# Kernel optimization log

Hardware: AMD Instinct MI355X
Metric: run time of the kernel (lower is better)

## Reference

```python
import jax, jax.numpy as jnp
import numpy as np

D_MODEL = 192
D_INNER = 384          # expand(2) * d_model
HEADDIM = 12
NHEADS = 32            # d_inner // headdim
DSTATE = 16
NGROUPS = 1
CONV_DIM = D_INNER + 2 * NGROUPS * DSTATE          # 416
D_IN_PROJ = 2 * D_INNER + 2 * NGROUPS * DSTATE + NHEADS  # 832
LN_EPS = 1e-5


def silu(x):
    return x * jax.nn.sigmoid(x)


def depthwise_conv2d(x_nchw, w, b):
    # groups == channels depthwise conv, kernel 3, padding 1 (SAME)
    out = jax.lax.conv_general_dilated(
        x_nchw, w, window_strides=(1, 1), padding='SAME',
        feature_group_count=CONV_DIM,
        dimension_numbers=('NCHW', 'OIHW', 'NCHW'))
    return out + b[None, :, None, None]


def setup_inputs() -> dict:
    key = jax.random.key(0)
    ks = jax.random.split(key, 10)
    Bn, H, W = 4, 128, 128
    u = jax.random.normal(ks[0], (Bn, H, W, D_MODEL), jnp.float32)
    t = jax.random.normal(ks[1], (Bn, H, W, D_MODEL), jnp.float32)
    s_in = 1.0 / np.sqrt(D_MODEL)
    W_in = jax.random.normal(ks[2], (D_IN_PROJ, D_MODEL), jnp.float32) * s_in
    W_t_in = jax.random.normal(ks[3], (D_IN_PROJ, D_MODEL), jnp.float32) * s_in
    conv_w = jax.random.normal(ks[4], (CONV_DIM, 1, 3, 3), jnp.float32) * (1.0 / 3.0)
    conv_b = jnp.zeros((CONV_DIM,), jnp.float32)
    # dt_bias = inverse-softplus of dt sampled log-uniform in [dt_min, dt_max]
    dt0 = jnp.exp(jax.random.uniform(ks[5], (NHEADS,)) * (np.log(0.1) - np.log(0.001)) + np.log(0.001))
    dt_bias = dt0 + jnp.log(-jnp.expm1(-dt0))
    A_log = jnp.log(jax.random.uniform(ks[6], (NHEADS,), minval=1.0, maxval=16.0))
    D = jnp.ones((NHEADS,), jnp.float32)
    ln_gamma = jnp.ones((D_INNER,), jnp.float32)
    ln_beta = jnp.zeros((D_INNER,), jnp.float32)
    W_out = jax.random.normal(ks[7], (D_MODEL, D_INNER), jnp.float32) * (1.0 / np.sqrt(D_INNER))
    return dict(u=u, t=t, W_in=W_in, W_t_in=W_t_in, conv_w=conv_w, conv_b=conv_b,
                dt_bias=dt_bias, A_log=A_log, D=D, ln_gamma=ln_gamma, ln_beta=ln_beta,
                W_out=W_out)


def reference(u, t, W_in, W_t_in, conv_w, conv_b, dt_bias, A_log, D,
              ln_gamma, ln_beta, W_out):
    B0, H, W_, C0 = u.shape
    L = H * W_
    uu = u.reshape(B0, L, C0)
    tt = t.reshape(B0, L, C0)

    # in_proj on main branch: split into z, xBC, dt
    zxbcdt = uu @ W_in.T                                    # (B, L, 832)
    z = zxbcdt[..., :D_INNER]                               # (B, L, 384)
    xBC = zxbcdt[..., D_INNER:D_INNER + CONV_DIM]           # (B, L, 416)
    dt = zxbcdt[..., D_INNER + CONV_DIM:]                   # (B, L, 32)
    dt = jax.nn.softplus(dt + dt_bias)

    # t branch: only x1B1C1 part is ultimately used (C := C1)
    x1B1C1 = (tt @ W_t_in.T)[..., D_INNER:D_INNER + CONV_DIM]

    # depthwise 3x3 conv + silu on both branches
    xBC = xBC.reshape(B0, H, W_, CONV_DIM).transpose(0, 3, 1, 2)
    xBC = silu(depthwise_conv2d(xBC, conv_w, conv_b))
    xBC = xBC.transpose(0, 2, 3, 1).reshape(B0, L, CONV_DIM)

    x1B1C1 = x1B1C1.reshape(B0, H, W_, CONV_DIM).transpose(0, 3, 1, 2)
    x1B1C1 = silu(depthwise_conv2d(x1B1C1, conv_w, conv_b))
    x1B1C1 = x1B1C1.transpose(0, 2, 3, 1).reshape(B0, L, CONV_DIM)

    x = xBC[..., :D_INNER]                                  # V features (B, L, 384)
    Bk = xBC[..., D_INNER:D_INNER + NGROUPS * DSTATE]       # K (B, L, 16)
    Cq = x1B1C1[..., D_INNER + NGROUPS * DSTATE:]           # Q from t-branch (B, L, 16)

    A = -jnp.exp(A_log)                                     # (nheads,), negative

    # non-causal linear attention duality (ngroups == 1)
    V = x.reshape(B0, L, NHEADS, HEADDIM).transpose(0, 2, 1, 3)   # (B, h, L, d)
    dtT = dt.transpose(0, 2, 1)                                   # (B, h, L)
    dA = -(dtT[..., None] * A[None, :, None, None])               # ssd_positve_dA: positive
    V_scaled = V * dA
    KV = jnp.einsum('bln,bhld->bhnd', Bk, V_scaled)               # (B, h, 16, 12)
    y = jnp.einsum('bln,bhnd->bhld', Cq, KV) + V * D[None, :, None, None]
    y = y.transpose(0, 2, 1, 3).reshape(B0, L, D_INNER)

    # LayerNorm over d_inner
    mu = jnp.mean(y, axis=-1, keepdims=True)
    var = jnp.mean((y - mu) ** 2, axis=-1, keepdims=True)
    y = (y - mu) * jax.lax.rsqrt(var + LN_EPS) * ln_gamma + ln_beta

    y = y * z
    out = y @ W_out.T
    return out.reshape(B0, H, W_, C0)
```

## Files before the change

kernel.cpp:

```cpp
#include <hip/hip_runtime.h>
#include <hip/hip_bf16.h>
#include <math.h>


#define BN 4
#define HH 128
#define WWID 128
#define LTOK (HH*WWID)
#define NTOK (BN*LTOK)
#define DMODEL 192
#define DINNER 384
#define NH 32
#define HD 12
#define DST 16
#define CONVD 416
#define KVCHUNKS 64
#define PM 256
#define TILE_SH 12288
#define TILE_BY 24576
#define TROW ((size_t)NTOK*64)

typedef __hip_bfloat16 bf16;
typedef unsigned int uint32;
typedef unsigned short ushort16;
typedef __attribute__((ext_vector_type(8))) short bf16x8;
typedef __attribute__((ext_vector_type(4))) float f32x4;
typedef __attribute__((ext_vector_type(16))) float f32x16;

__device__ __forceinline__ float bflo(uint32 v){ return __uint_as_float((v & 0xffffu) << 16); }
__device__ __forceinline__ float bfhi(uint32 v){ return __uint_as_float(v & 0xffff0000u); }
__device__ __forceinline__ ushort16 f2bf(float f){
    __hip_bfloat16 h = __float2bfloat16(f);
    return *reinterpret_cast<const ushort16*>(&h);
}
__device__ __forceinline__ float ldbf(const bf16* p){
    return __uint_as_float(((uint32)(*(const ushort16*)p)) << 16);
}
__device__ __forceinline__ float softplusf(float x){
    return (x > 20.f) ? x : log1pf(expf(x));
}
__device__ __forceinline__ float siluf(float x){
    return x / (1.f + expf(-x));
}

union BFPK { short s[8]; bf16x8 v; };

__global__ __launch_bounds__(256) void k_prep(
    const float* __restrict__ Win, const float* __restrict__ Wout,
    const float* __restrict__ cw,
    bf16* __restrict__ Wsw, bf16* __restrict__ Woutbf, float* __restrict__ wtr)
{
    const int i = blockIdx.x*256 + threadIdx.x;
    if (i < 832*DMODEL) {
        const int ch = i / DMODEL, k = i - ch*DMODEL;
        const int nt = ch >> 6, row = ch & 63;
        const int ks = k ^ ((row & 7) << 3);
        Wsw[(size_t)nt*TILE_SH + row*DMODEL + ks] = __float2bfloat16(Win[i]);
    }
    if (i < DMODEL*DINNER) Woutbf[i] = __float2bfloat16(Wout[i]);
    if (i < CONVD*9) { const int c = i/9, k = i - c*9; wtr[k*420 + c] = cw[i]; }
}

__global__ __launch_bounds__(512) void k_proj_mfma(
    const float* __restrict__ u, const bf16* __restrict__ Wsw,
    const float* __restrict__ dt_b, const float* __restrict__ A_log,
    bf16* __restrict__ z_bf, bf16* __restrict__ xbc_pre, float* __restrict__ dA)
{
    __shared__ __align__(16) short S[3*TILE_SH];

    const int tid = threadIdx.x;
    const int m0 = blockIdx.x * PM;
    const int ntbase = blockIdx.y * 7;
    const int ntiles = blockIdx.y ? 6 : 7;
    const int wid = tid >> 6, lane = tid & 63;
    const int fr = lane & 31;
    const int hi = lane >> 5;

    const char* gW = (const char*)Wsw;
    auto GLOAD = [&](int nt, int buf) {
        const char* src = gW + (size_t)nt*TILE_BY + wid*3072 + lane*16;
        char* dst = ((char*)S) + buf*TILE_BY + wid*3072;
        #pragma unroll
        for (int c = 0; c < 3; ++c)
            __builtin_amdgcn_global_load_lds(
                (const __attribute__((address_space(1))) void*)(src + c*1024),
                (__attribute__((address_space(3))) void*)(dst + c*1024), 16, 0, 0);
    };

    GLOAD(ntbase, 0);

    const float db = dt_b[fr];
    const float al = expf(A_log[fr]);
    bf16x8 a[12];
    {
        const float* arow = u + (size_t)(m0 + wid*32 + fr)*DMODEL;
        #pragma unroll
        for (int ks=0;ks<12;++ks) {
            const float4 a0 = *(const float4*)(arow + ks*16 + hi*8);
            const float4 a1 = *(const float4*)(arow + ks*16 + hi*8 + 4);
            BFPK pk;
            pk.s[0]=(short)f2bf(a0.x); pk.s[1]=(short)f2bf(a0.y);
            pk.s[2]=(short)f2bf(a0.z); pk.s[3]=(short)f2bf(a0.w);
            pk.s[4]=(short)f2bf(a1.x); pk.s[5]=(short)f2bf(a1.y);
            pk.s[6]=(short)f2bf(a1.z); pk.s[7]=(short)f2bf(a1.w);
            a[ks] = pk.v;
        }
    }
    asm volatile("s_waitcnt vmcnt(0)" ::: "memory");
    GLOAD(ntbase + 1, 1);
    __builtin_amdgcn_s_barrier();
    __builtin_amdgcn_sched_barrier(0);

    const int kswz = (fr & 7) << 3;

    for (int i = 0; i < ntiles; ++i) {
        const int nt = ntbase + i;
        const short* Sb = &S[(i % 3)*TILE_SH];

        f32x16 acc0, acc1;
        #pragma unroll
        for (int q=0;q<16;++q) { acc0[q]=0.f; acc1[q]=0.f; }

        #pragma unroll
        for (int ks=0;ks<12;++ks) {
            const int kk = (ks*16 + hi*8) ^ kswz;
            const bf16x8 b0 = *(const bf16x8*)&Sb[fr*DMODEL + kk];
            const bf16x8 b1 = *(const bf16x8*)&Sb[(32+fr)*DMODEL + kk];
            acc0 = __builtin_amdgcn_mfma_f32_32x32x16_bf16(a[ks], b0, acc0, 0, 0, 0);
            acc1 = __builtin_amdgcn_mfma_f32_32x32x16_bf16(a[ks], b1, acc1, 0, 0, 0);
        }

        #pragma unroll
        for (int ni=0;ni<2;++ni) {
            const f32x16& ac = ni ? acc1 : acc0;
            const int n0 = nt*64 + ni*32;
            if (n0 < DINNER) {
                bf16* dst = z_bf + (size_t)nt*TROW + (ni*32 + fr);
                #pragma unroll
                for (int r=0;r<16;++r) {
                    const int tok = m0 + wid*32 + (r&3) + 8*(r>>2) + 4*hi;
                    dst[(size_t)tok*64] = __float2bfloat16(ac[r]);
                }
            } else if (n0 < 800) {
                const int loc = n0 - DINNER + fr;
                bf16* dst = xbc_pre + (size_t)(loc>>6)*TROW + (loc & 63);
                #pragma unroll
                for (int r=0;r<16;++r) {
                    const int tok = m0 + wid*32 + (r&3) + 8*(r>>2) + 4*hi;
                    dst[(size_t)tok*64] = __float2bfloat16(ac[r]);
                }
            } else {
                #pragma unroll
                for (int r=0;r<16;++r) {
                    const int tok = m0 + wid*32 + (r&3) + 8*(r>>2) + 4*hi;
                    const float dt = softplusf(ac[r] + db);
                    dA[(size_t)tok*NH + fr] = dt * al;
                }
            }
        }

        if (i + 2 < ntiles) {
            GLOAD(nt + 2, (i + 2) % 3);
            asm volatile("s_waitcnt vmcnt(35)" ::: "memory");
        } else {
            asm volatile("s_waitcnt vmcnt(32)" ::: "memory");
        }
        __builtin_amdgcn_s_barrier();
        __builtin_amdgcn_sched_barrier(0);
    }
}

__global__ __launch_bounds__(256) void k_tproj(
    const float* __restrict__ t, const float* __restrict__ Wtin, float* __restrict__ cq_pre)
{
    __shared__ float ts[16][196];
    __shared__ float ws[16][196];
    const int tid = threadIdx.x;
    const int tok0 = blockIdx.x * 16;
    #pragma unroll
    for (int i = 0; i < 3; ++i) {
        const int flat = tid + 256*i;
        const int row = flat / 48, c = (flat % 48)*4;
        *(float4*)&ts[row][c] = *(const float4*)(t    + (size_t)(tok0+row)*DMODEL + c);
        *(float4*)&ws[row][c] = *(const float4*)(Wtin + (size_t)(784+row)*DMODEL + c);
    }
    __syncthreads();
    const int tt = tid >> 4, n = tid & 15;
    float s0=0.f,s1=0.f,s2=0.f,s3=0.f;
    #pragma unroll 4
    for (int k = 0; k < DMODEL; k += 4) {
        s0 = fmaf(ts[tt][k+0], ws[n][k+0], s0);
        s1 = fmaf(ts[tt][k+1], ws[n][k+1], s1);
        s2 = fmaf(ts[tt][k+2], ws[n][k+2], s2);
        s3 = fmaf(ts[tt][k+3], ws[n][k+3], s3);
    }
    cq_pre[(size_t)(tok0+tt)*DST + n] = (s0+s1)+(s2+s3);
}

__global__ __launch_bounds__(416) void k_conv416(
    const bf16* __restrict__ in, const float* __restrict__ wtr, const float* __restrict__ cb,
    bf16* __restrict__ out)
{
    __shared__ float ws[9*420];
    __shared__ float bs[416];
    const int tid = threadIdx.x;
    for (int i = tid; i < 9*420; i += 416) ws[i] = wtr[i];
    if (tid < 416) bs[tid] = cb[tid];
    __syncthreads();

    const int pl  = tid / 52;
    const int grp = tid - pl*52;
    const int c0  = grp*8;
    const int pix = blockIdx.x*8 + pl;
    const int hw  = pix & (LTOK-1);
    const int h = hw >> 7, w = hw & 127;
    const int bb = pix >> 14;

    const bf16* inT = in + (size_t)(c0 >> 6)*TROW + (c0 & 63);

    float acc[8];
    {
        const float4 b0 = *(const float4*)&bs[c0];
        const float4 b1 = *(const float4*)&bs[c0+4];
        acc[0]=b0.x; acc[1]=b0.y; acc[2]=b0.z; acc[3]=b0.w;
        acc[4]=b1.x; acc[5]=b1.y; acc[6]=b1.z; acc[7]=b1.w;
    }

    #pragma unroll
    for (int dh=-1; dh<=1; ++dh) {
        const int hh = h + dh;
        if ((unsigned)hh >= (unsigned)HH) continue;
        #pragma unroll
        for (int dw=-1; dw<=1; ++dw) {
            const int w2 = w + dw;
            if ((unsigned)w2 >= (unsigned)WWID) continue;
            const int wi = (dh+1)*3 + (dw+1);
            const int pix2 = (bb<<14) + (hh<<7) + w2;
            const uint4 v = *(const uint4*)((const ushort16*)inT + (size_t)pix2*64);
            const float4 w0 = *(const float4*)&ws[wi*420 + c0];
            const float4 w1 = *(const float4*)&ws[wi*420 + c0 + 4];
            acc[0] = fmaf(bflo(v.x), w0.x, acc[0]);
            acc[1] = fmaf(bfhi(v.x), w0.y, acc[1]);
            acc[2] = fmaf(bflo(v.y), w0.z, acc[2]);
            acc[3] = fmaf(bfhi(v.y), w0.w, acc[3]);
            acc[4] = fmaf(bflo(v.z), w1.x, acc[4]);
            acc[5] = fmaf(bfhi(v.z), w1.y, acc[5]);
            acc[6] = fmaf(bflo(v.w), w1.z, acc[6]);
            acc[7] = fmaf(bfhi(v.w), w1.w, acc[7]);
        }
    }

    uint4 o;
    o.x = ((uint32)f2bf(siluf(acc[1])) << 16) | (uint32)f2bf(siluf(acc[0]));
    o.y = ((uint32)f2bf(siluf(acc[3])) << 16) | (uint32)f2bf(siluf(acc[2]));
    o.z = ((uint32)f2bf(siluf(acc[5])) << 16) | (uint32)f2bf(siluf(acc[4]));
    o.w = ((uint32)f2bf(siluf(acc[7])) << 16) | (uint32)f2bf(siluf(acc[6]));
    *(uint4*)((ushort16*)out + (size_t)pix*CONVD + c0) = o;
}

__global__ __launch_bounds__(256) void k_conv16(
    const float* __restrict__ in, const float* __restrict__ cw, const float* __restrict__ cb,
    bf16* __restrict__ out)
{
    const int idx = blockIdx.x*256 + threadIdx.x;
    const int cc = idx & 15;
    const int pix = idx >> 4;
    const int hw = pix & (LTOK-1);
    const int h = hw >> 7, w = hw & 127;
    const int bb = pix >> 14;
    const int c = 400 + cc;

    float wg[9];
    #pragma unroll
    for (int k=0;k<9;++k) wg[k] = cw[c*9+k];
    float a = cb[c];
    #pragma unroll
    for (int dh=-1; dh<=1; ++dh) {
        const int hh = h + dh;
        if ((unsigned)hh >= (unsigned)HH) continue;
        #pragma unroll
        for (int dw=-1; dw<=1; ++dw) {
            const int w2 = w + dw;
            if ((unsigned)w2 >= (unsigned)WWID) continue;
            a = fmaf(in[((size_t)((bb<<14)+(hh<<7)+w2))*16 + cc], wg[(dh+1)*3 + (dw+1)], a);
        }
    }
    out[(size_t)pix*16 + cc] = __float2bfloat16(siluf(a));
}

__global__ __launch_bounds__(512) void k_kv(
    const bf16* __restrict__ xbc_post, const float* __restrict__ dA,
    float* __restrict__ partial)
{
    __shared__ short vsb[16][408];
    __shared__ float das[16][32];
    const int tid = threadIdx.x;
    const int b = blockIdx.y;
    const int n = tid & 15;
    const int g = tid >> 4;

    float acc[12];
    #pragma unroll
    for (int j=0;j<12;++j) acc[j]=0.f;

    const int l0base = b*LTOK + blockIdx.x*256;

    for (int it = 0; it < 16; ++it) {
        const int l0 = l0base + it*16;
        for (int i = tid; i < 16*200; i += 512) {
            const int tok = i / 200;
            const int c2 = i - tok*200;
            const uint32 v = *(const uint32*)((const ushort16*)xbc_post
                                + (size_t)(l0+tok)*CONVD + c2*2);
            *(uint32*)&vsb[tok][c2*2] = v;
        }
        {
            const int tok = tid >> 5, h = tid & 31;
            das[tok][h] = dA[(size_t)(l0+tok)*NH + h];
        }
        __syncthreads();

        #pragma unroll
        for (int tok = 0; tok < 16; ++tok) {
            const uint32 bkraw = (uint32)(ushort16)vsb[tok][DINNER + n];
            const float s = __uint_as_float(bkraw << 16) * das[tok][g];
            const uint32* vp = (const uint32*)&vsb[tok][g*12];
            const uint32 w0 = vp[0], w1 = vp[1], w2 = vp[2];
            acc[0]  = fmaf(s, bflo(w0), acc[0]);
            acc[1]  = fmaf(s, bfhi(w0), acc[1]);
            acc[2]  = fmaf(s, bflo(w1), acc[2]);
            acc[3]  = fmaf(s, bfhi(w1), acc[3]);
            acc[4]  = fmaf(s, bflo(w2), acc[4]);
            acc[5]  = fmaf(s, bfhi(w2), acc[5]);
            const uint32* vq = (const uint32*)&vsb[tok][g*12 + 6];
            const uint32 w3 = vq[0], w4 = vq[1], w5 = vq[2];
            acc[6]  = fmaf(s, bflo(w3), acc[6]);
            acc[7]  = fmaf(s, bfhi(w3), acc[7]);
            acc[8]  = fmaf(s, bflo(w4), acc[8]);
            acc[9]  = fmaf(s, bfhi(w4), acc[9]);
            acc[10] = fmaf(s, bflo(w5), acc[10]);
            acc[11] = fmaf(s, bfhi(w5), acc[11]);
        }
        __syncthreads();
    }

    float* dst = partial + ((size_t)(b*KVCHUNKS + blockIdx.x))*6144 + (size_t)tid*12;
    #pragma unroll
    for (int j4=0;j4<3;++j4)
        *(float4*)(dst + j4*4) = make_float4(acc[j4*4], acc[j4*4+1], acc[j4*4+2], acc[j4*4+3]);
}

__global__ __launch_bounds__(256) void k_kvred(
    const float* __restrict__ partial, float* __restrict__ kv)
{
    const int idx = blockIdx.x*256 + threadIdx.x;
    const int b = idx / 6144;
    const int flat = idx - b*6144;
    const float* p = partial + (size_t)(b*KVCHUNKS)*6144 + flat;
    float s = 0.f;
    #pragma unroll 4
    for (int c = 0; c < KVCHUNKS; ++c) s += p[(size_t)c*6144];
    kv[idx] = s;
}

__global__ __launch_bounds__(256) void k_ynorm(
    const bf16* __restrict__ xbc_post, const bf16* __restrict__ cq_bf,
    const bf16* __restrict__ z_bf, const float* __restrict__ kv,
    const float* __restrict__ Dv, const float* __restrict__ ln_g, const float* __restrict__ ln_b,
    bf16* __restrict__ yz)
{
    __shared__ __align__(16) short kvb[24*64*8];
    __shared__ float gs[DINNER], bs2[DINNER], ds[DINNER];
    const int tid = threadIdx.x;
    const int token0 = blockIdx.x * 64;
    const int b = token0 >> 14;
    const float* kvB = kv + (size_t)b*6144;

    for (int i = tid; i < DINNER; i += 256) {
        gs[i]  = ln_g[i];
        bs2[i] = ln_b[i];
        ds[i]  = Dv[i/HD];
    }
    #pragma unroll
    for (int it = 0; it < 6; ++it) {
        const int f = tid + 256*it;
        const int t = f >> 6, l = f & 63;
        const int q = l >> 4;
        const int nb = (q & 1)*8;
        const int hd = t*16 + (l & 15);
        const int h = hd/HD, d = hd - h*HD;
        const float* src = kvB + (size_t)h*192 + d;
        BFPK pk;
        #pragma unroll
        for (int i = 0; i < 8; ++i) {
            const float v = src[(size_t)(nb+i)*12];
            if (q < 2) {
                pk.s[i] = (short)f2bf(v);
            } else {
                const uint32 hb = (uint32)(ushort16)f2bf(v);
                pk.s[i] = (short)f2bf(v - __uint_as_float(hb << 16));
            }
        }
        *(bf16x8*)&kvb[(size_t)f*8] = pk.v;
    }
    __syncthreads();

    const int wid = tid >> 6, lane = tid & 63;
    const int fr = lane & 15, fq = lane >> 4;
    const int tokA = token0 + wid*16;

    const bf16x8 cqf = *(const bf16x8*)((const short*)cq_bf + (size_t)(tokA+fr)*DST + (fq&1)*8);

    f32x4 acc[24];
    #pragma unroll
    for (int t = 0; t < 24; ++t) {
        const bf16x8 bfv = *(const bf16x8*)&kvb[(t*64 + lane)*8];
        f32x4 z4 = (f32x4){0.f,0.f,0.f,0.f};
        acc[t] = __builtin_amdgcn_mfma_f32_16x16x32_bf16(cqf, bfv, z4, 0, 0, 0);
    }

    const int tokj0 = tokA + fq*4;
    float s[4]  = {0.f,0.f,0.f,0.f};
    float s2[4] = {0.f,0.f,0.f,0.f};
    #pragma unroll
    for (int t = 0; t < 24; ++t) {
        const int hd = t*16 + fr;
        const float dvh = ds[hd];
        #pragma unroll
        for (int j = 0; j < 4; ++j) {
            const float vv = ldbf(xbc_post + (size_t)(tokj0+j)*CONVD + hd);
            const float y = fmaf(vv, dvh, acc[t][j]);
            acc[t][j] = y;
            s[j] += y;
            s2[j] = fmaf(y, y, s2[j]);
        }
    }
    #pragma unroll
    for (int j = 0; j < 4; ++j) {
        #pragma unroll
        for (int off = 8; off > 0; off >>= 1) {
            s[j]  += __shfl_xor(s[j],  off, 16);
            s2[j] += __shfl_xor(s2[j], off, 16);
        }
    }
    float mu[4], rs[4];
    #pragma unroll
    for (int j = 0; j < 4; ++j) {
        mu[j] = s[j] * (1.f/384.f);
        const float var = s2[j]*(1.f/384.f) - mu[j]*mu[j];
        rs[j] = rsqrtf(var + 1e-5f);
    }

    #pragma unroll
    for (int t = 0; t < 24; ++t) {
        const int hd = t*16 + fr;
        const float g = gs[hd], be = bs2[hd];
        const bf16* zsrc = z_bf + (size_t)(hd>>6)*TROW + (hd & 63);
        #pragma unroll
        for (int j = 0; j < 4; ++j) {
            const int tok = tokj0 + j;
            const float yn = fmaf((acc[t][j] - mu[j])*rs[j], g, be);
            const float zv = ldbf(zsrc + (size_t)tok*64);
            yz[(size_t)tok*DINNER + hd] = __float2bfloat16(yn*zv);
        }
    }
}

__global__ __launch_bounds__(256) void k_out_mfma(
    const bf16* __restrict__ yz, const bf16* __restrict__ Wbf, float* __restrict__ out)
{
    __shared__ __align__(16) short As[2][128*40];
    __shared__ __align__(16) short Bs[2][192*40];

    const int tid = threadIdx.x;
    const int m0 = blockIdx.x * 128;
    const int wid = tid >> 6, lane = tid & 63;
    const int wm = wid >> 1, wn = wid & 1;
    const int fr = lane & 15, fq = lane >> 4;

    const int arow = tid >> 1, ahalf = tid & 1;
    auto stageA = [&](int ks, int buf) {
        const short* g = (const short*)yz + (size_t)(m0 + arow)*DINNER + ks*32 + ahalf*16;
        const uint4 v0 = *(const uint4*)g;
        const uint4 v1 = *(const uint4*)(g + 8);
        short* d = &As[buf][arow*40 + ahalf*16];
        *(uint4*)d = v0;
        *(uint4*)(d + 8) = v1;
    };
    auto stageB = [&](int ks, int buf) {
        #pragma unroll
        for (int i = 0; i < 3; ++i) {
            const int flat = tid + 256*i;
            const int row = flat >> 2, q = flat & 3;
            const uint4 v = *(const uint4*)((const short*)Wbf + (size_t)row*DINNER + ks*32 + q*8);
            *(uint4*)&Bs[buf][row*40 + q*8] = v;
        }
    };

    f32x4 acc[4][6];
    #pragma unroll
    for (int mi=0;mi<4;++mi)
        #pragma unroll
        for (int ni=0;ni<6;++ni) acc[mi][ni] = (f32x4){0.f,0.f,0.f,0.f};

    stageA(0, 0); stageB(0, 0);
    __syncthreads();

    const int aoff = (wm*64 + fr)*40 + fq*8;
    const int boff = (wn*96 + fr)*40 + fq*8;

    #pragma unroll
    for (int ks = 0; ks < 12; ++ks) {
        const int cur = ks & 1;
        if (ks < 11) { stageA(ks+1, cur^1); stageB(ks+1, cur^1); }
        bf16x8 a[4], b[6];
        #pragma unroll
        for (int mi=0;mi<4;++mi) a[mi] = *(const bf16x8*)(&As[cur][aoff + mi*640]);
        #pragma unroll
        for (int ni=0;ni<6;++ni) b[ni] = *(const bf16x8*)(&Bs[cur][boff + ni*640]);
        #pragma unroll
        for (int mi=0;mi<4;++mi)
            #pragma unroll
            for (int ni=0;ni<6;++ni)
                acc[mi][ni] = __builtin_amdgcn_mfma_f32_16x16x32_bf16(a[mi], b[ni], acc[mi][ni], 0, 0, 0);
        __syncthreads();
    }

    #pragma unroll
    for (int mi=0;mi<4;++mi) {
        #pragma unroll
        for (int j=0;j<4;++j) {
            const int tok = m0 + wm*64 + mi*16 + fq*4 + j;
            #pragma unroll
            for (int ni=0;ni<6;++ni) {
                const int n = wn*96 + ni*16 + fr;
                out[(size_t)tok*DMODEL + n] = acc[mi][ni][j];
            }
        }
    }
}

extern "C" void kernel_launch(void* const* d_in, const int* in_sizes, int n_in,
                              void* d_out, int out_size, void* d_ws, size_t ws_size,
                              hipStream_t stream)
{
    const float* u      = (const float*)d_in[0];
    const float* t      = (const float*)d_in[1];
    const float* Win    = (const float*)d_in[2];
    const float* Wtin   = (const float*)d_in[3];
    const float* conv_w = (const float*)d_in[4];
    const float* conv_b = (const float*)d_in[5];
    const float* dt_b   = (const float*)d_in[6];
    const float* A_log  = (const float*)d_in[7];
    const float* Dv     = (const float*)d_in[8];
    const float* ln_g   = (const float*)d_in[9];
    const float* ln_bt  = (const float*)d_in[10];
    const float* W_out  = (const float*)d_in[11];
    float* out = (float*)d_out;

    char* p = (char*)d_ws;
    bf16* z_bf     = (bf16*)p;  p += (size_t)6*TROW*2;
    bf16* xbc_pre  = (bf16*)p;  p += (size_t)7*TROW*2;
    bf16* xbc_post = (bf16*)p;  p += (size_t)NTOK*CONVD*2;
    float* cq_pre  = (float*)p; p += (size_t)NTOK*DST*4;
    bf16* cq_bf    = (bf16*)p;  p += (size_t)NTOK*DST*2;
    float* dA      = (float*)p; p += (size_t)NTOK*NH*4;
    bf16* yz       = (bf16*)p;  p += (size_t)NTOK*DINNER*2;
    float* kv      = (float*)p; p += (size_t)BN*NH*DST*HD*4;
    bf16* Wsw      = (bf16*)p;  p += (size_t)832*DMODEL*2;
    bf16* Wout_bf  = (bf16*)p;  p += (size_t)DMODEL*DINNER*2;
    float* wtr     = (float*)p; p += (size_t)9*420*4;

    float* kv_part = (float*)xbc_pre;

    k_prep<<<624, 256, 0, stream>>>(Win, W_out, conv_w, Wsw, Wout_bf, wtr);
    k_proj_mfma<<<dim3(NTOK/PM, 2), 512, 0, stream>>>(u, Wsw, dt_b, A_log, z_bf, xbc_pre, dA);
    k_tproj<<<NTOK/16, 256, 0, stream>>>(t, Wtin, cq_pre);
    k_conv416<<<NTOK/8, 416, 0, stream>>>(xbc_pre, wtr, conv_b, xbc_post);
    k_conv16<<<NTOK*16/256, 256, 0, stream>>>(cq_pre, conv_w, conv_b, cq_bf);
    k_kv<<<dim3(KVCHUNKS, BN), 512, 0, stream>>>(xbc_post, dA, kv_part);
    k_kvred<<<BN*6144/256, 256, 0, stream>>>(kv_part, kv);
    k_ynorm<<<NTOK/64, 256, 0, stream>>>(xbc_post, cq_bf, z_bf, kv,
                                         Dv, ln_g, ln_bt, yz);
    k_out_mfma<<<512, 256, 0, stream>>>(yz, Wout_bf, out);
}
```

Measured before the change: 321.6 us.

## Fuse output projection into layernorm kernel via shared-memory yz tile

Merges the output projection GEMM into the y/LayerNorm kernel. Each block keeps its 64x384 bf16 gated activations in padded LDS and runs MFMA against a W_out that is pre-swizzled into per-lane fragment order. The fused kernel reads B fragments directly from global/L2. This removes the yz intermediate write and re-read in HBM and one launch, at the cost of larger LDS use, more registers, and repeated weight reads from cache by every block.

Measured after the change: 307.9 us. 4.3% less time.

```diff
diff --git a/kernel.cpp b/kernel.cpp
--- a/kernel.cpp
+++ b/kernel.cpp
@@ -19,6 +19,7 @@
 #define TILE_SH 12288
 #define TILE_BY 24576
 #define TROW ((size_t)NTOK*64)
+#define YPAD 392
 
 typedef __hip_bfloat16 bf16;
 typedef unsigned int uint32;
@@ -48,7 +49,7 @@
 __global__ __launch_bounds__(256) void k_prep(
     const float* __restrict__ Win, const float* __restrict__ Wout,
     const float* __restrict__ cw,
-    bf16* __restrict__ Wsw, bf16* __restrict__ Woutbf, float* __restrict__ wtr)
+    bf16* __restrict__ Wsw, bf16* __restrict__ Wout_sh, float* __restrict__ wtr)
 {
     const int i = blockIdx.x*256 + threadIdx.x;
     if (i < 832*DMODEL) {
@@ -57,7 +58,13 @@
         const int ks = k ^ ((row & 7) << 3);
         Wsw[(size_t)nt*TILE_SH + row*DMODEL + ks] = __float2bfloat16(Win[i]);
     }
-    if (i < DMODEL*DINNER) Woutbf[i] = __float2bfloat16(Wout[i]);
+    if (i < DMODEL*DINNER) {
+        const int m = i / DINNER, k = i - m*DINNER;
+        const int ni = m >> 4, mr = m & 15;
+        const int ks = k >> 5, kq = (k >> 3) & 3, ii = k & 7;
+        const int lane = kq*16 + mr;
+        Wout_sh[(size_t)((ni*12 + ks)*64 + lane)*8 + ii] = __float2bfloat16(Wout[i]);
+    }
     if (i < CONVD*9) { const int c = i/9, k = i - c*9; wtr[k*420 + c] = cw[i]; }
 }
 
@@ -363,13 +370,14 @@
     kv[idx] = s;
 }
 
-__global__ __launch_bounds__(256) void k_ynorm(
+__global__ __launch_bounds__(256) void k_ynorm_out(
     const bf16* __restrict__ xbc_post, const bf16* __restrict__ cq_bf,
     const bf16* __restrict__ z_bf, const float* __restrict__ kv,
     const float* __restrict__ Dv, const float* __restrict__ ln_g, const float* __restrict__ ln_b,
-    bf16* __restrict__ yz)
+    const bf16* __restrict__ Wout_sh, float* __restrict__ out)
 {
     __shared__ __align__(16) short kvb[24*64*8];
+    __shared__ __align__(16) short yzs[64*YPAD];
     __shared__ float gs[DINNER], bs2[DINNER], ds[DINNER];
     const int tid = threadIdx.x;
     const int token0 = blockIdx.x * 64;
@@ -461,82 +469,36 @@
             const int tok = tokj0 + j;
             const float yn = fmaf((acc[t][j] - mu[j])*rs[j], g, be);
             const float zv = ldbf(zsrc + (size_t)tok*64);
-            yz[(size_t)tok*DINNER + hd] = __float2bfloat16(yn*zv);
-        }
-    }
-}
-
-__global__ __launch_bounds__(256) void k_out_mfma(
-    const bf16* __restrict__ yz, const bf16* __restrict__ Wbf, float* __restrict__ out)
-{
-    __shared__ __align__(16) short As[2][128*40];
-    __shared__ __align__(16) short Bs[2][192*40];
-
-    const int tid = threadIdx.x;
-    const int m0 = blockIdx.x * 128;
-    const int wid = tid >> 6, lane = tid & 63;
-    const int wm = wid >> 1, wn = wid & 1;
-    const int fr = lane & 15, fq = lane >> 4;
-
-    const int arow = tid >> 1, ahalf = tid & 1;
-    auto stageA = [&](int ks, int buf) {
-        const short* g = (const short*)yz + (size_t)(m0 + arow)*DINNER + ks*32 + ahalf*16;
-        const uint4 v0 = *(const uint4*)g;
-        const uint4 v1 = *(const uint4*)(g + 8);
-        short* d = &As[buf][arow*40 + ahalf*16];
-        *(uint4*)d = v0;
-        *(uint4*)(d + 8) = v1;
-    };
-    auto stageB = [&](int ks, int buf) {
-        #pragma unroll
-        for (int i = 0; i < 3; ++i) {
-            const int flat = tid + 256*i;
-            const int row = flat >> 2, q = flat & 3;
-            const uint4 v = *(const uint4*)((const short*)Wbf + (size_t)row*DINNER + ks*32 + q*8);
-            *(uint4*)&Bs[buf][row*40 + q*8] = v;
-        }
-    };
-
-    f32x4 acc[4][6];
-    #pragma unroll
-    for (int mi=0;mi<4;++mi)
-        #pragma unroll
-        for (int ni=0;ni<6;++ni) acc[mi][ni] = (f32x4){0.f,0.f,0.f,0.f};
-
-    stageA(0, 0); stageB(0, 0);
-    __syncthreads();
-
-    const int aoff = (wm*64 + fr)*40 + fq*8;
-    const int boff = (wn*96 + fr)*40 + fq*8;
+            yzs[(wid*16 + fq*4 + j)*YPAD + hd] = (short)f2bf(yn*zv);
+        }
+    }
+
+    const short* yrow = &yzs[(wid*16 + fr)*YPAD];
+    bf16x8 af[12];
+    #pragma unroll
+    for (int ks = 0; ks < 12; ++ks)
+        af[ks] = *(const bf16x8*)(yrow + ks*32 + fq*8);
+
+    f32x4 oacc[12];
+    #pragma unroll
+    for (int ni = 0; ni < 12; ++ni) oacc[ni] = (f32x4){0.f,0.f,0.f,0.f};
 
     #pragma unroll
     for (int ks = 0; ks < 12; ++ks) {
-        const int cur = ks & 1;
-        if (ks < 11) { stageA(ks+1, cur^1); stageB(ks+1, cur^1); }
-        bf16x8 a[4], b[6];
-        #pragma unroll
-        for (int mi=0;mi<4;++mi) a[mi] = *(const bf16x8*)(&As[cur][aoff + mi*640]);
-        #pragma unroll
-        for (int ni=0;ni<6;++ni) b[ni] = *(const bf16x8*)(&Bs[cur][boff + ni*640]);
-        #pragma unroll
-        for (int mi=0;mi<4;++mi)
-            #pragma unroll
-            for (int ni=0;ni<6;++ni)
-                acc[mi][ni] = __builtin_amdgcn_mfma_f32_16x16x32_bf16(a[mi], b[ni], acc[mi][ni], 0, 0, 0);
-        __syncthreads();
-    }
-
-    #pragma unroll
-    for (int mi=0;mi<4;++mi) {
-        #pragma unroll
-        for (int j=0;j<4;++j) {
-            const int tok = m0 + wm*64 + mi*16 + fq*4 + j;
-            #pragma unroll
-            for (int ni=0;ni<6;++ni) {
-                const int n = wn*96 + ni*16 + fr;
-                out[(size_t)tok*DMODEL + n] = acc[mi][ni][j];
-            }
-        }
+        #pragma unroll
+        for (int ni = 0; ni < 12; ++ni) {
+            const bf16x8 bw = *(const bf16x8*)((const short*)Wout_sh
+                                + (size_t)((ni*12 + ks)*64 + lane)*8);
+            oacc[ni] = __builtin_amdgcn_mfma_f32_16x16x32_bf16(af[ks], bw, oacc[ni], 0, 0, 0);
+        }
+    }
+
+    #pragma unroll
+    for (int ni = 0; ni < 12; ++ni) {
+        const int n = ni*16 + fr;
+        #pragma unroll
+        for (int r = 0; r < 4; ++r)
+            out[(size_t)(tokj0 + r)*DMODEL + n] = oacc[ni][r];
     }
 }
 
@@ -565,22 +527,20 @@
     float* cq_pre  = (float*)p; p += (size_t)NTOK*DST*4;
     bf16* cq_bf    = (bf16*)p;  p += (size_t)NTOK*DST*2;
     float* dA      = (float*)p; p += (size_t)NTOK*NH*4;
-    bf16* yz       = (bf16*)p;  p += (size_t)NTOK*DINNER*2;
     float* kv      = (float*)p; p += (size_t)BN*NH*DST*HD*4;
     bf16* Wsw      = (bf16*)p;  p += (size_t)832*DMODEL*2;
-    bf16* Wout_bf  = (bf16*)p;  p += (size_t)DMODEL*DINNER*2;
+    bf16* Wout_sh  = (bf16*)p;  p += (size_t)DMODEL*DINNER*2;
     float* wtr     = (float*)p; p += (size_t)9*420*4;
 
     float* kv_part = (float*)xbc_pre;
 
-    k_prep<<<624, 256, 0, stream>>>(Win, W_out, conv_w, Wsw, Wout_bf, wtr);
+    k_prep<<<624, 256, 0, stream>>>(Win, W_out, conv_w, Wsw, Wout_sh, wtr);
     k_proj_mfma<<<dim3(NTOK/PM, 2), 512, 0, stream>>>(u, Wsw, dt_b, A_log, z_bf, xbc_pre, dA);
     k_tproj<<<NTOK/16, 256, 0, stream>>>(t, Wtin, cq_pre);
     k_conv416<<<NTOK/8, 416, 0, stream>>>(xbc_pre, wtr, conv_b, xbc_post);
     k_conv16<<<NTOK*16/256, 256, 0, stream>>>(cq_pre, conv_w, conv_b, cq_bf);
     k_kv<<<dim3(KVCHUNKS, BN), 512, 0, stream>>>(xbc_post, dA, kv_part);
     k_kvred<<<BN*6144/256, 256, 0, stream>>>(kv_part, kv);
-    k_ynorm<<<NTOK/64, 256, 0, stream>>>(xbc_post, cq_bf, z_bf, kv,
-                                         Dv, ln_g, ln_bt, yz);
-    k_out_mfma<<<512, 256, 0, stream>>>(yz, Wout_bf, out);
-}
+    k_ynorm_out<<<NTOK/64, 256, 0, stream>>>(xbc_post, cq_bf, z_bf, kv,
+                                             Dv, ln_g, ln_bt, Wout_sh, out);
+}
```
